# Optimization experiments

Hardware: AMD Instinct MI355X
Metric: run time of the kernel (lower is better)

Reference implementation:

```python
import jax, jax.numpy as jnp
import numpy as np

D_MODEL = 512
N_HEADS = 8
HEAD_DIM = D_MODEL // N_HEADS
KV_RANK = 128
B, T = 8, 4096


def _rope(x):
    # x: (B, H, T, D); non-interleaved half rotation as in the source
    d = x.shape[-1]
    half = d // 2
    freq = 1.0 / (10000.0 ** (jnp.arange(half, dtype=jnp.float32) / half))
    t = jnp.arange(x.shape[2], dtype=jnp.float32)
    freqs = jnp.einsum('i,j->ij', t, freq)          # (T, half)
    cos_f = jnp.cos(freqs)[None, None, :, :]
    sin_f = jnp.sin(freqs)[None, None, :, :]
    x1, x2 = jnp.split(x, 2, axis=-1)
    return jnp.concatenate([x1 * cos_f - x2 * sin_f, x1 * sin_f + x2 * cos_f], axis=-1)


def setup_inputs() -> dict:
    key = jax.random.key(0)
    ks = jax.random.split(key, 9)
    s = lambda fan_in: 1.0 / np.sqrt(fan_in)
    return {
        'x':  jax.random.normal(ks[0], (B, T, D_MODEL), dtype=jnp.float32),
        'Wq': jax.random.normal(ks[1], (D_MODEL, D_MODEL), dtype=jnp.float32) * s(D_MODEL),
        'bq': jnp.zeros((D_MODEL,), dtype=jnp.float32),
        'Wd': jax.random.normal(ks[2], (D_MODEL, KV_RANK), dtype=jnp.float32) * s(D_MODEL),
        'bd': jnp.zeros((KV_RANK,), dtype=jnp.float32),
        'Wu': jax.random.normal(ks[3], (KV_RANK, D_MODEL * 2), dtype=jnp.float32) * s(KV_RANK),
        'bu': jnp.zeros((D_MODEL * 2,), dtype=jnp.float32),
        'Wo': jax.random.normal(ks[4], (D_MODEL, D_MODEL), dtype=jnp.float32) * s(D_MODEL),
        'bo': jnp.zeros((D_MODEL,), dtype=jnp.float32),
    }


def reference(x, Wq, bq, Wd, bd, Wu, bu, Wo, bo):
    b, t, _ = x.shape
    q = (x @ Wq + bq).reshape(b, t, N_HEADS, HEAD_DIM).transpose(0, 2, 1, 3)   # (B,H,T,D)
    kv = ((x @ Wd + bd) @ Wu + bu).reshape(b, t, N_HEADS, 2 * HEAD_DIM)
    k, v = jnp.split(kv, 2, axis=-1)
    k = k.transpose(0, 2, 1, 3)                                                # (B,H,T,D)
    v = v.transpose(0, 2, 1, 3)
    q = jax.nn.elu(_rope(q)) + 1.0
    k = jax.nn.elu(_rope(k)) + 1.0
    context = jnp.einsum('bhtd,bhte->bhde', k, v)      # (B,H,D,D)
    out = jnp.einsum('bhtd,bhde->bhte', q, context)    # (B,H,T,D)
    k_sum = k.sum(axis=2)                              # (B,H,D)
    z = 1.0 / (jnp.einsum('bhtd,bhd->bht', q, k_sum) + 1e-6)
    out = out * z[..., None]
    out = out.transpose(0, 2, 1, 3).reshape(b, t, D_MODEL)
    return out @ Wo + bo
```

## Files before the change

### kernel.cpp

```cpp
#include <hip/hip_runtime.h>
#include <math.h>

#define T_SEQ 4096
#define BATCH 8
#define DM    512
#define NH    8
#define HD    64
#define RANK  128
#define NCHUNK 16
#define MTOT  (BATCH * T_SEQ)
#define BK 64

typedef unsigned int u32;
typedef unsigned short u16;
using bf16x8  = __attribute__((ext_vector_type(8))) __bf16;
using floatx4 = __attribute__((ext_vector_type(4))) float;

__device__ __forceinline__ u16 f2bf(float f) {
  u32 u = __float_as_uint(f);
  u32 r = (u + 0x7FFFu + ((u >> 16) & 1u)) >> 16;
  return (u16)r;
}
__device__ __forceinline__ void hilo(float f, u16& h, u16& l) {
  h = f2bf(f);
  float hf = __uint_as_float(((u32)h) << 16);
  l = f2bf(f - hf);
}
__device__ __forceinline__ float elu1(float x) {
  return (x > 0.f) ? x + 1.f : expf(x);
}
__device__ __forceinline__ void async16(void* lds, const void* g) {
  __builtin_amdgcn_global_load_lds(
      (const __attribute__((address_space(1))) u32*)g,
      (__attribute__((address_space(3))) u32*)lds, 16, 0, 0);
}
__device__ __forceinline__ bf16x8 fragld(const u16* base, int row, int kk, int quad) {
  int ch = (kk * 4 + quad) ^ (row & 7);
  return *(const bf16x8*)((const char*)base + row * 128 + ch * 16);
}
__device__ __forceinline__ bf16x8 fragldA(const u16* base, int row, int gc) {
  int ch = gc ^ (row & 7);
  return *(const bf16x8*)((const char*)base + row * 256 + ch * 16);
}

__global__ void cs_kernel(float2* __restrict__ cs) {
  int i = blockIdx.x * 256 + threadIdx.x;
  if (i >= T_SEQ * 32) return;
  int t = i >> 5, d = i & 31;
  double freq = pow(10000.0, -(double)d / 32.0);
  double a = (double)t * freq;
  cs[i] = make_float2((float)cos(a), (float)sin(a));
}

__global__ __launch_bounds__(256) void pack_bf16(const float* __restrict__ x,
                                                 u16* __restrict__ y) {
  int i = blockIdx.x * 256 + threadIdx.x;
  const float4 v = ((const float4*)x)[i];
  ushort4 o;
  o.x = f2bf(v.x); o.y = f2bf(v.y); o.z = f2bf(v.z); o.w = f2bf(v.w);
  ((ushort4*)y)[i] = o;
}

__global__ __launch_bounds__(256) void transpose_cast(const float* __restrict__ W,
                                                      u16* __restrict__ WT,
                                                      int K, int N) {
  __shared__ float t[32][33];
  int kb = blockIdx.x * 32, nb = blockIdx.y * 32;
  int tx = threadIdx.x & 31, tg = threadIdx.x >> 5;
#pragma unroll
  for (int i = 0; i < 4; i++)
    t[tg * 4 + i][tx] = W[(size_t)(kb + tg * 4 + i) * N + nb + tx];
  __syncthreads();
#pragma unroll
  for (int i = 0; i < 4; i++)
    WT[(size_t)(nb + tg * 4 + i) * K + kb + tx] = f2bf(t[tx][tg * 4 + i]);
}

__global__ __launch_bounds__(256) void transpose_cast_hilo(
    const float* __restrict__ W, u16* __restrict__ WTh, u16* __restrict__ WTl,
    int K, int N) {
  __shared__ float t[32][33];
  int kb = blockIdx.x * 32, nb = blockIdx.y * 32;
  int tx = threadIdx.x & 31, tg = threadIdx.x >> 5;
#pragma unroll
  for (int i = 0; i < 4; i++)
    t[tg * 4 + i][tx] = W[(size_t)(kb + tg * 4 + i) * N + nb + tx];
  __syncthreads();
#pragma unroll
  for (int i = 0; i < 4; i++) {
    u16 h, l;
    hilo(t[tx][tg * 4 + i], h, l);
    WTh[(size_t)(nb + tg * 4 + i) * K + kb + tx] = h;
    WTl[(size_t)(nb + tg * 4 + i) * K + kb + tx] = l;
  }
}

template <bool BF16OUT>
__global__ __launch_bounds__(256) void gemm_bf16_bt(
    const u16* __restrict__ A, const u16* __restrict__ BT,
    const float* __restrict__ bias, void* __restrict__ Cv,
    int M, int N, int K) {
  __shared__ u16 As[128 * BK];
  __shared__ u16 Bs[128 * BK];
  const int tid = threadIdx.x;
  const int lane = tid & 63, w = tid >> 6;
  const int m0 = blockIdx.y * 128, n0 = blockIdx.x * 128;
  const int wm = (w & 1) * 64, wn = (w >> 1) * 64;
  const int srow = lane >> 3, schunk = lane & 7;
  const int lane15 = lane & 15, quad = lane >> 4;
  floatx4 acc[4][4] = {};
  for (int kt = 0; kt < K; kt += BK) {
    __syncthreads();
#pragma unroll
    for (int i = 0; i < 4; i++) {
      int R = (w * 4 + i) * 8 + srow;
      int cg = schunk ^ (R & 7);
      async16((char*)As + (w * 4 + i) * 1024,
              (const char*)A + ((size_t)(m0 + R) * K + kt) * 2 + cg * 16);
      async16((char*)Bs + (w * 4 + i) * 1024,
              (const char*)BT + ((size_t)(n0 + R) * K + kt) * 2 + cg * 16);
    }
    __syncthreads();
#pragma unroll
    for (int kk = 0; kk < 2; kk++) {
      bf16x8 af[4], bfr[4];
#pragma unroll
      for (int mi = 0; mi < 4; mi++) af[mi] = fragld(As, wm + mi * 16 + lane15, kk, quad);
#pragma unroll
      for (int ni = 0; ni < 4; ni++) bfr[ni] = fragld(Bs, wn + ni * 16 + lane15, kk, quad);
#pragma unroll
      for (int mi = 0; mi < 4; mi++)
#pragma unroll
        for (int ni = 0; ni < 4; ni++)
          acc[mi][ni] = __builtin_amdgcn_mfma_f32_16x16x32_bf16(
              af[mi], bfr[ni], acc[mi][ni], 0, 0, 0);
    }
  }
#pragma unroll
  for (int mi = 0; mi < 4; mi++) {
    int row = m0 + wm + mi * 16 + (quad << 2);
#pragma unroll
    for (int ni = 0; ni < 4; ni++) {
      int col = n0 + wn + ni * 16 + lane15;
      float bb = bias[col];
#pragma unroll
      for (int r = 0; r < 4; r++) {
        float v = acc[mi][ni][r] + bb;
        if (BF16OUT) ((u16*)Cv)[(size_t)(row + r) * N + col] = f2bf(v);
        else         ((float*)Cv)[(size_t)(row + r) * N + col] = v;
      }
    }
  }
}

__global__ __launch_bounds__(256) void gemm_wd_hilo(
    const u16* __restrict__ A, const u16* __restrict__ BT,
    const float* __restrict__ bias, u16* __restrict__ Ch, u16* __restrict__ Cl,
    int M, int N, int K) {
  __shared__ u16 As[128 * BK];
  __shared__ u16 Bs[128 * BK];
  const int tid = threadIdx.x;
  const int lane = tid & 63, w = tid >> 6;
  const int m0 = blockIdx.y * 128, n0 = blockIdx.x * 128;
  const int wm = (w & 1) * 64, wn = (w >> 1) * 64;
  const int srow = lane >> 3, schunk = lane & 7;
  const int lane15 = lane & 15, quad = lane >> 4;
  floatx4 acc[4][4] = {};
  for (int kt = 0; kt < K; kt += BK) {
    __syncthreads();
#pragma unroll
    for (int i = 0; i < 4; i++) {
      int R = (w * 4 + i) * 8 + srow;
      int cg = schunk ^ (R & 7);
      async16((char*)As + (w * 4 + i) * 1024,
              (const char*)A + ((size_t)(m0 + R) * K + kt) * 2 + cg * 16);
      async16((char*)Bs + (w * 4 + i) * 1024,
              (const char*)BT + ((size_t)(n0 + R) * K + kt) * 2 + cg * 16);
    }
    __syncthreads();
#pragma unroll
    for (int kk = 0; kk < 2; kk++) {
      bf16x8 af[4], bfr[4];
#pragma unroll
      for (int mi = 0; mi < 4; mi++) af[mi] = fragld(As, wm + mi * 16 + lane15, kk, quad);
#pragma unroll
      for (int ni = 0; ni < 4; ni++) bfr[ni] = fragld(Bs, wn + ni * 16 + lane15, kk, quad);
#pragma unroll
      for (int mi = 0; mi < 4; mi++)
#pragma unroll
        for (int ni = 0; ni < 4; ni++)
          acc[mi][ni] = __builtin_amdgcn_mfma_f32_16x16x32_bf16(
              af[mi], bfr[ni], acc[mi][ni], 0, 0, 0);
    }
  }
#pragma unroll
  for (int mi = 0; mi < 4; mi++) {
    int row = m0 + wm + mi * 16 + (quad << 2);
#pragma unroll
    for (int ni = 0; ni < 4; ni++) {
      int col = n0 + wn + ni * 16 + lane15;
      float bb = bias[col];
#pragma unroll
      for (int r = 0; r < 4; r++) {
        float v = acc[mi][ni][r] + bb;
        u16 hh, ll;
        hilo(v, hh, ll);
        size_t idx = (size_t)(row + r) * N + col;
        Ch[idx] = hh;
        Cl[idx] = ll;
      }
    }
  }
}

__global__ __launch_bounds__(256, 3) void ctx_fused(
    const u16* __restrict__ Chi, const u16* __restrict__ Clo,
    const u16* __restrict__ Wuh, const u16* __restrict__ Wul,
    const float* __restrict__ bu, const float2* __restrict__ cs,
    float* __restrict__ ctxp, float* __restrict__ ksump) {
  __shared__ __align__(16) u16 Ah_[32 * 128];
  __shared__ __align__(16) u16 Al_[32 * 128];
  __shared__ __align__(16) u16 Kh_[64 * 64], Kl_[64 * 64];
  __shared__ __align__(16) u16 Vh_[64 * 64], Vl_[64 * 64];
  __shared__ float bus[128];
  __shared__ float ksl[256];
  const int tid = threadIdx.x;
  const int lane = tid & 63, w = tid >> 6;
  const int lane15 = lane & 15, quad = lane >> 4;
  const int chunk = blockIdx.x, bh = blockIdx.y;
  const int b = bh >> 3, h = bh & 7;
  if (tid < 128) bus[tid] = bu[h * RANK + tid];

  bf16x8 wuh[2][2][2], wul[2][2][2];
  {
    const int cb = (w >> 1) * 4 + (w & 1);
#pragma unroll
    for (int rp = 0; rp < 2; rp++)
#pragma unroll
      for (int kk = 0; kk < 2; kk++)
#pragma unroll
        for (int ct = 0; ct < 2; ct++) {
          size_t off = (size_t)(h * 128 + (cb + ct * 2) * 16 + lane15) * RANK
                       + rp * 64 + kk * 32 + quad * 8;
          wuh[rp][kk][ct] = *(const bf16x8*)(Wuh + off);
          wul[rp][kk][ct] = *(const bf16x8*)(Wul + off);
        }
  }

  const int t00 = chunk * (T_SEQ / NCHUNK);
  auto stageA = [&](int tg0) {
#pragma unroll
    for (int i = 0; i < 2; i++) {
      int R = i * 16 + w * 4 + (lane >> 4);
      int cg = (lane & 15) ^ (R & 7);
      size_t aoff = ((size_t)(b * T_SEQ + tg0 + R) * RANK + cg * 8) * 2;
      async16((char*)Ah_ + (i * 16 + w * 4) * 256, (const char*)Chi + aoff);
      async16((char*)Al_ + (i * 16 + w * 4) * 256, (const char*)Clo + aoff);
    }
  };

  floatx4 acc2[4] = {};
  float ks0 = 0.f, ks1 = 0.f;
  stageA(t00);
  for (int tile = 0; tile < T_SEQ / NCHUNK / 64; tile++) {
    const int t0 = t00 + tile * 64;
#pragma unroll
    for (int hh = 0; hh < 2; hh++) {
      __syncthreads();
      floatx4 acc[2][2] = {};
#pragma unroll
      for (int rp = 0; rp < 2; rp++)
#pragma unroll
        for (int kk = 0; kk < 2; kk++) {
          const int gc = rp * 8 + kk * 4 + quad;
          bf16x8 ah[2], al[2];
#pragma unroll
          for (int tt = 0; tt < 2; tt++) {
            ah[tt] = fragldA(Ah_, tt * 16 + lane15, gc);
            al[tt] = fragldA(Al_, tt * 16 + lane15, gc);
          }
#pragma unroll
          for (int tt = 0; tt < 2; tt++)
#pragma unroll
            for (int ct = 0; ct < 2; ct++) {
              acc[tt][ct] = __builtin_amdgcn_mfma_f32_16x16x32_bf16(
                  ah[tt], wuh[rp][kk][ct], acc[tt][ct], 0, 0, 0);
              acc[tt][ct] = __builtin_amdgcn_mfma_f32_16x16x32_bf16(
                  ah[tt], wul[rp][kk][ct], acc[tt][ct], 0, 0, 0);
              acc[tt][ct] = __builtin_amdgcn_mfma_f32_16x16x32_bf16(
                  al[tt], wuh[rp][kk][ct], acc[tt][ct], 0, 0, 0);
            }
        }
      __syncthreads();
      if (hh == 0) stageA(t0 + 32);
      else if (tile < T_SEQ / NCHUNK / 64 - 1) stageA(t0 + 64);
      const int tbase = t0 + hh * 32;
      if (w < 2) {
        const int d = w * 16 + lane15;
        const float b1 = bus[d], b2 = bus[d + 32];
#pragma unroll
        for (int tt = 0; tt < 2; tt++) {
          const int tg = tbase + tt * 16 + (quad << 2);
          ushort4 khl, kll, khh, klh;
          float s0 = 0.f, s1 = 0.f;
#pragma unroll
          for (int r = 0; r < 4; r++) {
            float2 sc = cs[(size_t)(tg + r) * 32 + d];
            float x1 = acc[tt][0][r] + b1;
            float x2 = acc[tt][1][r] + b2;
            float k1 = elu1(x1 * sc.x - x2 * sc.y);
            float k2 = elu1(x1 * sc.y + x2 * sc.x);
            s0 += k1; s1 += k2;
            u16 hh_, ll_;
            hilo(k1, hh_, ll_); ((u16*)&khl)[r] = hh_; ((u16*)&kll)[r] = ll_;
            hilo(k2, hh_, ll_); ((u16*)&khh)[r] = hh_; ((u16*)&klh)[r] = ll_;
          }
          ks0 += s0; ks1 += s1;
          const int chq = hh * 4 + tt * 2 + (quad >> 1);
          const int off = d * 128 + (((chq ^ (d & 7)) << 4) | ((quad & 1) << 3));
          *(ushort4*)((char*)Kh_ + off)            = khl;
          *(ushort4*)((char*)Kl_ + off)            = kll;
          *(ushort4*)((char*)Kh_ + off + 32 * 128) = khh;
          *(ushort4*)((char*)Kl_ + off + 32 * 128) = klh;
        }
      } else {
        const int e = (w - 2) * 16 + lane15;
#pragma unroll
        for (int ct = 0; ct < 2; ct++) {
          const float be = bus[64 + e + ct * 32];
#pragma unroll
          for (int tt = 0; tt < 2; tt++) {
            ushort4 vh4, vl4;
#pragma unroll
            for (int r = 0; r < 4; r++) {
              u16 hh_, ll_;
              hilo(acc[tt][ct][r] + be, hh_, ll_);
              ((u16*)&vh4)[r] = hh_; ((u16*)&vl4)[r] = ll_;
            }
            const int chq = hh * 4 + tt * 2 + (quad >> 1);
            const int off = (e + ct * 32) * 128 +
                            (((chq ^ (e & 7)) << 4) | ((quad & 1) << 3));
            *(ushort4*)((char*)Vh_ + off) = vh4;
            *(ushort4*)((char*)Vl_ + off) = vl4;
          }
        }
      }
    }
    __syncthreads();
#pragma unroll
    for (int kk = 0; kk < 2; kk++) {
      bf16x8 kh8 = fragld(Kh_, w * 16 + lane15, kk, quad);
      bf16x8 kl8 = fragld(Kl_, w * 16 + lane15, kk, quad);
#pragma unroll
      for (int ni = 0; ni < 4; ni++) {
        bf16x8 vh8 = fragld(Vh_, ni * 16 + lane15, kk, quad);
        bf16x8 vl8 = fragld(Vl_, ni * 16 + lane15, kk, quad);
        acc2[ni] = __builtin_amdgcn_mfma_f32_16x16x32_bf16(kh8, vh8, acc2[ni], 0, 0, 0);
        acc2[ni] = __builtin_amdgcn_mfma_f32_16x16x32_bf16(kh8, vl8, acc2[ni], 0, 0, 0);
        acc2[ni] = __builtin_amdgcn_mfma_f32_16x16x32_bf16(kl8, vh8, acc2[ni], 0, 0, 0);
      }
    }
  }
  const size_t obase = ((size_t)bh * NCHUNK + chunk) * 4096;
#pragma unroll
  for (int ni = 0; ni < 4; ni++)
#pragma unroll
    for (int r = 0; r < 4; r++)
      ctxp[obase + (size_t)(w * 16 + (quad << 2) + r) * 64 + ni * 16 + lane15] = acc2[ni][r];
  if (w < 2) {
    ksl[w * 128 + lane]      = ks0;
    ksl[w * 128 + 64 + lane] = ks1;
  }
  __syncthreads();
  if (tid < 64) {
    const int d = tid;
    const int wk = (d >> 4) & 1, hi = d >> 5, l15 = d & 15;
    float s = 0.f;
#pragma unroll
    for (int q = 0; q < 4; q++) s += ksl[wk * 128 + hi * 64 + q * 16 + l15];
    ksump[(bh * NCHUNK + chunk) * 64 + d] = s;
  }
}

__global__ __launch_bounds__(256) void reduce_kernel(
    const float* __restrict__ ctxp, const float* __restrict__ ksump,
    float* __restrict__ ctx, float* __restrict__ ksum) {
  int bh = blockIdx.x, tid = threadIdx.x;
  for (int i = tid; i < 4096; i += 256) {
    float s = 0.f;
    for (int c = 0; c < NCHUNK; c++) s += ctxp[(size_t)(bh * NCHUNK + c) * 4096 + i];
    ctx[(size_t)bh * 4096 + i] = s;
  }
  if (tid < 64) {
    float s = 0.f;
    for (int c = 0; c < NCHUNK; c++) s += ksump[(bh * NCHUNK + c) * 64 + tid];
    ksum[bh * 64 + tid] = s;
  }
}

__global__ __launch_bounds__(256) void out_kernel(
    const float* __restrict__ Q, const float* __restrict__ ctx,
    const float* __restrict__ ksum, const float2* __restrict__ cs,
    u16* __restrict__ attn) {
  __shared__ __align__(16) float Qs[128 * 68];
  __shared__ __align__(16) float Cts[64 * 68];
  __shared__ float ks[64];
  __shared__ float zs[128];
  const int tid = threadIdx.x;
  const int tt0 = blockIdx.x * 128;
  const int bh = blockIdx.y;
  const int b = bh >> 3, h = bh & 7;
  for (int i = tid; i < 4096; i += 256)
    Cts[(i >> 6) * 68 + (i & 63)] = ctx[(size_t)bh * 4096 + i];
  if (tid < 64) ks[tid] = ksum[bh * 64 + tid];
  for (int i = tid; i < 8192; i += 256) {
    int t = i >> 6, d = i & 63;
    Qs[t * 68 + d] = Q[(size_t)(b * T_SEQ + tt0 + t) * DM + h * HD + d];
  }
  __syncthreads();
  for (int i = tid; i < 128 * 32; i += 256) {
    int t = i >> 5, d = i & 31;
    float x1 = Qs[t * 68 + d], x2 = Qs[t * 68 + d + 32];
    float2 sc = cs[(size_t)(tt0 + t) * 32 + d];
    float r1 = x1 * sc.x - x2 * sc.y;
    float r2 = x1 * sc.y + x2 * sc.x;
    Qs[t * 68 + d]      = (r1 > 0.f) ? r1 + 1.f : expf(r1);
    Qs[t * 68 + d + 32] = (r2 > 0.f) ? r2 + 1.f : expf(r2);
  }
  __syncthreads();
  if (tid < 128) {
    float z = 0.f;
#pragma unroll 8
    for (int d = 0; d < 64; d++) z += Qs[tid * 68 + d] * ks[d];
    zs[tid] = 1.f / (z + 1e-6f);
  }
  __syncthreads();
  const int tx = tid & 15, ty = tid >> 4;
  float acc[8][4] = {};
  for (int d = 0; d < 64; d++) {
    const float4 c4 = *(const float4*)&Cts[d * 68 + tx * 4];
#pragma unroll
    for (int i = 0; i < 8; i++) {
      float q = Qs[(ty * 8 + i) * 68 + d];
      acc[i][0] += q * c4.x; acc[i][1] += q * c4.y;
      acc[i][2] += q * c4.z; acc[i][3] += q * c4.w;
    }
  }
#pragma unroll
  for (int i = 0; i < 8; i++) {
    int t = ty * 8 + i;
    float zz = zs[t];
    ushort4 o;
    o.x = f2bf(acc[i][0] * zz); o.y = f2bf(acc[i][1] * zz);
    o.z = f2bf(acc[i][2] * zz); o.w = f2bf(acc[i][3] * zz);
    *(ushort4*)&attn[(size_t)(b * T_SEQ + tt0 + t) * DM + h * HD + tx * 4] = o;
  }
}

extern "C" void kernel_launch(void* const* d_in, const int* in_sizes, int n_in,
                              void* d_out, int out_size, void* d_ws, size_t ws_size,
                              hipStream_t stream) {
  const float* x  = (const float*)d_in[0];
  const float* Wq = (const float*)d_in[1];
  const float* bq = (const float*)d_in[2];
  const float* Wd = (const float*)d_in[3];
  const float* bd = (const float*)d_in[4];
  const float* Wu = (const float*)d_in[5];
  const float* bu = (const float*)d_in[6];
  const float* Wo = (const float*)d_in[7];
  const float* bo = (const float*)d_in[8];
  float* out = (float*)d_out;

  float* ws = (float*)d_ws;
  size_t o_cs   = 0;
  size_t o_Q    = o_cs + (size_t)T_SEQ * 32 * 2;
  size_t o_Chi  = o_Q + (size_t)MTOT * DM;
  size_t o_Clo  = o_Chi + (size_t)MTOT * RANK / 2;
  size_t o_ksp  = o_Clo + (size_t)MTOT * RANK / 2;
  size_t o_ctx  = o_ksp + (size_t)64 * NCHUNK * 64;
  size_t o_ks   = o_ctx + (size_t)64 * 4096;
  size_t o_xbf  = o_ks + 64 * 64;
  size_t o_wqT  = o_xbf + (size_t)MTOT * DM / 2;
  size_t o_wdT  = o_wqT + (size_t)DM * DM / 2;
  size_t o_woT  = o_wdT + (size_t)DM * RANK / 2;
  size_t o_wuTh = o_woT + (size_t)DM * DM / 2;
  size_t o_wuTl = o_wuTh + (size_t)(2 * DM) * RANK / 2;
  size_t total  = o_wuTl + (size_t)(2 * DM) * RANK / 2;
  if (ws_size < total * sizeof(float)) return;

  float2* cs  = (float2*)(ws + o_cs);
  float* Qb   = ws + o_Q;
  u16* Chi    = (u16*)(ws + o_Chi);
  u16* Clo    = (u16*)(ws + o_Clo);
  float* ksp  = ws + o_ksp;
  float* ctxf = ws + o_ctx;
  float* ksf  = ws + o_ks;
  u16* x_bf   = (u16*)(ws + o_xbf);
  u16* attn_bf= x_bf;
  float* ctxp = ws + o_xbf;
  u16* WqT    = (u16*)(ws + o_wqT);
  u16* WdT    = (u16*)(ws + o_wdT);
  u16* WoT    = (u16*)(ws + o_woT);
  u16* WuTh   = (u16*)(ws + o_wuTh);
  u16* WuTl   = (u16*)(ws + o_wuTl);

  cs_kernel<<<(T_SEQ * 32 + 255) / 256, 256, 0, stream>>>(cs);
  pack_bf16<<<(MTOT * DM / 4) / 256, 256, 0, stream>>>(x, x_bf);
  transpose_cast<<<dim3(DM / 32, DM / 32), 256, 0, stream>>>(Wq, WqT, DM, DM);
  transpose_cast<<<dim3(DM / 32, RANK / 32), 256, 0, stream>>>(Wd, WdT, DM, RANK);
  transpose_cast<<<dim3(DM / 32, DM / 32), 256, 0, stream>>>(Wo, WoT, DM, DM);
  transpose_cast_hilo<<<dim3(RANK / 32, (2 * DM) / 32), 256, 0, stream>>>(
      Wu, WuTh, WuTl, RANK, 2 * DM);

  gemm_bf16_bt<false><<<dim3(DM / 128, MTOT / 128), 256, 0, stream>>>(
      x_bf, WqT, bq, Qb, MTOT, DM, DM);
  gemm_wd_hilo<<<dim3(RANK / 128, MTOT / 128), 256, 0, stream>>>(
      x_bf, WdT, bd, Chi, Clo, MTOT, RANK, DM);
  ctx_fused<<<dim3(NCHUNK, BATCH * NH), 256, 0, stream>>>(
      Chi, Clo, WuTh, WuTl, bu, cs, ctxp, ksp);
  reduce_kernel<<<BATCH * NH, 256, 0, stream>>>(ctxp, ksp, ctxf, ksf);
  out_kernel<<<dim3(T_SEQ / 128, BATCH * NH), 256, 0, stream>>>(Qb, ctxf, ksf, cs, attn_bf);
  gemm_bf16_bt<false><<<dim3(DM / 128, MTOT / 128), 256, 0, stream>>>(
      attn_bf, WoT, bo, out, MTOT, DM, DM);
}
```

Measured before the change: 324.7 us.

## Halve ctx_fused K/V LDS tiles to 32 timesteps and raise occupancy to 4

The context kernel now builds K/V tiles of 32 timesteps instead of 64. It accumulates the K^T V product after every 32-row phase, which halves the K/V shared memory. The bias array moves from shared memory into per-lane registers, and the launch bound goes from 3 to 4 blocks per CU to get more waves resident. In exchange there are more barriers per token, and tighter register pressure could cause spills.

```diff
diff --git a/kernel.cpp b/kernel.cpp
--- a/kernel.cpp
+++ b/kernel.cpp
@@ -41,6 +41,10 @@
 __device__ __forceinline__ bf16x8 fragldA(const u16* base, int row, int gc) {
   int ch = gc ^ (row & 7);
   return *(const bf16x8*)((const char*)base + row * 256 + ch * 16);
+}
+__device__ __forceinline__ bf16x8 fragldK(const u16* base, int row, int quad) {
+  int ch = quad ^ (row & 3);
+  return *(const bf16x8*)((const char*)base + row * 64 + ch * 16);
 }
 
 __global__ void cs_kernel(float2* __restrict__ cs) {
@@ -213,23 +217,30 @@
   }
 }
 
-__global__ __launch_bounds__(256, 3) void ctx_fused(
+__global__ __launch_bounds__(256, 4) void ctx_fused(
     const u16* __restrict__ Chi, const u16* __restrict__ Clo,
     const u16* __restrict__ Wuh, const u16* __restrict__ Wul,
     const float* __restrict__ bu, const float2* __restrict__ cs,
     float* __restrict__ ctxp, float* __restrict__ ksump) {
   __shared__ __align__(16) u16 Ah_[32 * 128];
   __shared__ __align__(16) u16 Al_[32 * 128];
-  __shared__ __align__(16) u16 Kh_[64 * 64], Kl_[64 * 64];
-  __shared__ __align__(16) u16 Vh_[64 * 64], Vl_[64 * 64];
-  __shared__ float bus[128];
+  __shared__ __align__(16) u16 Kh_[64 * 32], Kl_[64 * 32];
+  __shared__ __align__(16) u16 Vh_[64 * 32], Vl_[64 * 32];
   __shared__ float ksl[256];
   const int tid = threadIdx.x;
   const int lane = tid & 63, w = tid >> 6;
   const int lane15 = lane & 15, quad = lane >> 4;
   const int chunk = blockIdx.x, bh = blockIdx.y;
   const int b = bh >> 3, h = bh & 7;
-  if (tid < 128) bus[tid] = bu[h * RANK + tid];
+
+  float b1 = 0.f, b2 = 0.f, be0 = 0.f, be1 = 0.f;
+  if (w < 2) {
+    b1 = bu[h * RANK + w * 16 + lane15];
+    b2 = bu[h * RANK + w * 16 + lane15 + 32];
+  } else {
+    be0 = bu[h * RANK + 64 + (w - 2) * 16 + lane15];
+    be1 = bu[h * RANK + 64 + (w - 2) * 16 + lane15 + 32];
+  }
 
   bf16x8 wuh[2][2][2], wul[2][2][2];
   {
@@ -262,99 +273,92 @@
   floatx4 acc2[4] = {};
   float ks0 = 0.f, ks1 = 0.f;
   stageA(t00);
-  for (int tile = 0; tile < T_SEQ / NCHUNK / 64; tile++) {
-    const int t0 = t00 + tile * 64;
-#pragma unroll
-    for (int hh = 0; hh < 2; hh++) {
-      __syncthreads();
-      floatx4 acc[2][2] = {};
-#pragma unroll
-      for (int rp = 0; rp < 2; rp++)
-#pragma unroll
-        for (int kk = 0; kk < 2; kk++) {
-          const int gc = rp * 8 + kk * 4 + quad;
-          bf16x8 ah[2], al[2];
-#pragma unroll
-          for (int tt = 0; tt < 2; tt++) {
-            ah[tt] = fragldA(Ah_, tt * 16 + lane15, gc);
-            al[tt] = fragldA(Al_, tt * 16 + lane15, gc);
+  for (int ph = 0; ph < 8; ph++) {
+    const int th0 = t00 + ph * 32;
+    __syncthreads();
+    floatx4 acc[2][2] = {};
+#pragma unroll
+    for (int rp = 0; rp < 2; rp++)
+#pragma unroll
+      for (int kk = 0; kk < 2; kk++) {
+        const int gc = rp * 8 + kk * 4 + quad;
+        bf16x8 ah[2], al[2];
+#pragma unroll
+        for (int tt = 0; tt < 2; tt++) {
+          ah[tt] = fragldA(Ah_, tt * 16 + lane15, gc);
+          al[tt] = fragldA(Al_, tt * 16 + lane15, gc);
+        }
+#pragma unroll
+        for (int tt = 0; tt < 2; tt++)
+#pragma unroll
+          for (int ct = 0; ct < 2; ct++) {
+            acc[tt][ct] = __builtin_amdgcn_mfma_f32_16x16x32_bf16(
+                ah[tt], wuh[rp][kk][ct], acc[tt][ct], 0, 0, 0);
+            acc[tt][ct] = __builtin_amdgcn_mfma_f32_16x16x32_bf16(
+                ah[tt], wul[rp][kk][ct], acc[tt][ct], 0, 0, 0);
+            acc[tt][ct] = __builtin_amdgcn_mfma_f32_16x16x32_bf16(
+                al[tt], wuh[rp][kk][ct], acc[tt][ct], 0, 0, 0);
           }
-#pragma unroll
-          for (int tt = 0; tt < 2; tt++)
-#pragma unroll
-            for (int ct = 0; ct < 2; ct++) {
-              acc[tt][ct] = __builtin_amdgcn_mfma_f32_16x16x32_bf16(
-                  ah[tt], wuh[rp][kk][ct], acc[tt][ct], 0, 0, 0);
-              acc[tt][ct] = __builtin_amdgcn_mfma_f32_16x16x32_bf16(
-                  ah[tt], wul[rp][kk][ct], acc[tt][ct], 0, 0, 0);
-              acc[tt][ct] = __builtin_amdgcn_mfma_f32_16x16x32_bf16(
-                  al[tt], wuh[rp][kk][ct], acc[tt][ct], 0, 0, 0);
-            }
+      }
+    __syncthreads();
+    if (ph < 7) stageA(th0 + 32);
+    if (w < 2) {
+      const int d = w * 16 + lane15;
+#pragma unroll
+      for (int tt = 0; tt < 2; tt++) {
+        const int tg = th0 + tt * 16 + (quad << 2);
+        ushort4 khl, kll, khh, klh;
+        float s0 = 0.f, s1 = 0.f;
+#pragma unroll
+        for (int r = 0; r < 4; r++) {
+          float2 sc = cs[(size_t)(tg + r) * 32 + d];
+          float x1 = acc[tt][0][r] + b1;
+          float x2 = acc[tt][1][r] + b2;
+          float k1 = elu1(x1 * sc.x - x2 * sc.y);
+          float k2 = elu1(x1 * sc.y + x2 * sc.x);
+          s0 += k1; s1 += k2;
+          u16 hh_, ll_;
+          hilo(k1, hh_, ll_); ((u16*)&khl)[r] = hh_; ((u16*)&kll)[r] = ll_;
+          hilo(k2, hh_, ll_); ((u16*)&khh)[r] = hh_; ((u16*)&klh)[r] = ll_;
         }
-      __syncthreads();
-      if (hh == 0) stageA(t0 + 32);
-      else if (tile < T_SEQ / NCHUNK / 64 - 1) stageA(t0 + 64);
-      const int tbase = t0 + hh * 32;
-      if (w < 2) {
-        const int d = w * 16 + lane15;
-        const float b1 = bus[d], b2 = bus[d + 32];
+        ks0 += s0; ks1 += s1;
+        const int chq = tt * 2 + (quad >> 1);
+        const int off = d * 64 + (((chq ^ (d & 3)) << 4) | ((quad & 1) << 3));
+        *(ushort4*)((char*)Kh_ + off)           = khl;
+        *(ushort4*)((char*)Kl_ + off)           = kll;
+        *(ushort4*)((char*)Kh_ + off + 32 * 64) = khh;
+        *(ushort4*)((char*)Kl_ + off + 32 * 64) = klh;
+      }
+    } else {
+      const int e = (w - 2) * 16 + lane15;
+#pragma unroll
+      for (int ct = 0; ct < 2; ct++) {
+        const float be = ct ? be1 : be0;
+        const int row = e + ct * 32;
 #pragma unroll
         for (int tt = 0; tt < 2; tt++) {
-          const int tg = tbase + tt * 16 + (quad << 2);
-          ushort4 khl, kll, khh, klh;
-          float s0 = 0.f, s1 = 0.f;
+          ushort4 vh4, vl4;
 #pragma unroll
           for (int r = 0; r < 4; r++) {
-            float2 sc = cs[(size_t)(tg + r) * 32 + d];
-            float x1 = acc[tt][0][r] + b1;
-            float x2 = acc[tt][1][r] + b2;
-            float k1 = elu1(x1 * sc.x - x2 * sc.y);
-            float k2 = elu1(x1 * sc.y + x2 * sc.x);
-            s0 += k1; s1 += k2;
             u16 hh_, ll_;
-            hilo(k1, hh_, ll_); ((u16*)&khl)[r] = hh_; ((u16*)&kll)[r] = ll_;
-            hilo(k2, hh_, ll_); ((u16*)&khh)[r] = hh_; ((u16*)&klh)[r] = ll_;
+            hilo(acc[tt][ct][r] + be, hh_, ll_);
+            ((u16*)&vh4)[r] = hh_; ((u16*)&vl4)[r] = ll_;
           }
-          ks0 += s0; ks1 += s1;
-          const int chq = hh * 4 + tt * 2 + (quad >> 1);
-          const int off = d * 128 + (((chq ^ (d & 7)) << 4) | ((quad & 1) << 3));
-          *(ushort4*)((char*)Kh_ + off)            = khl;
-          *(ushort4*)((char*)Kl_ + off)            = kll;
-          *(ushort4*)((char*)Kh_ + off + 32 * 128) = khh;
-          *(ushort4*)((char*)Kl_ + off + 32 * 128) = klh;
-        }
-      } else {
-        const int e = (w - 2) * 16 + lane15;
-#pragma unroll
-        for (int ct = 0; ct < 2; ct++) {
-          const float be = bus[64 + e + ct * 32];
-#pragma unroll
-          for (int tt = 0; tt < 2; tt++) {
-            ushort4 vh4, vl4;
-#pragma unroll
-            for (int r = 0; r < 4; r++) {
-              u16 hh_, ll_;
-              hilo(acc[tt][ct][r] + be, hh_, ll_);
-              ((u16*)&vh4)[r] = hh_; ((u16*)&vl4)[r] = ll_;
-            }
-            const int chq = hh * 4 + tt * 2 + (quad >> 1);
-            const int off = (e + ct * 32) * 128 +
-                            (((chq ^ (e & 7)) << 4) | ((quad & 1) << 3));
-            *(ushort4*)((char*)Vh_ + off) = vh4;
-            *(ushort4*)((char*)Vl_ + off) = vl4;
-          }
+          const int chq = tt * 2 + (quad >> 1);
+          const int off = row * 64 + (((chq ^ (row & 3)) << 4) | ((quad & 1) << 3));
+          *(ushort4*)((char*)Vh_ + off) = vh4;
+          *(ushort4*)((char*)Vl_ + off) = vl4;
         }
       }
     }
     __syncthreads();
-#pragma unroll
-    for (int kk = 0; kk < 2; kk++) {
-      bf16x8 kh8 = fragld(Kh_, w * 16 + lane15, kk, quad);
-      bf16x8 kl8 = fragld(Kl_, w * 16 + lane15, kk, quad);
+    {
+      bf16x8 kh8 = fragldK(Kh_, w * 16 + lane15, quad);
+      bf16x8 kl8 = fragldK(Kl_, w * 16 + lane15, quad);
 #pragma unroll
       for (int ni = 0; ni < 4; ni++) {
-        bf16x8 vh8 = fragld(Vh_, ni * 16 + lane15, kk, quad);
-        bf16x8 vl8 = fragld(Vl_, ni * 16 + lane15, kk, quad);
+        bf16x8 vh8 = fragldK(Vh_, ni * 16 + lane15, quad);
+        bf16x8 vl8 = fragldK(Vl_, ni * 16 + lane15, quad);
         acc2[ni] = __builtin_amdgcn_mfma_f32_16x16x32_bf16(kh8, vh8, acc2[ni], 0, 0, 0);
         acc2[ni] = __builtin_amdgcn_mfma_f32_16x16x32_bf16(kh8, vl8, acc2[ni], 0, 0, 0);
         acc2[ni] = __builtin_amdgcn_mfma_f32_16x16x32_bf16(kl8, vh8, acc2[ni], 0, 0, 0);
```

After: 354.9 us. 1.09x slower.
